# Performance work log

Hardware: AMD Instinct MI355X
Metric: run time of the kernel (lower is better)

Reference implementation:

```python
import jax, jax.numpy as jnp
import numpy as np

D_IN = 1024
D_OUT = 1024
SEQ = 4096


def setup_inputs() -> dict:
    key = jax.random.key(0)
    kx, kq, kk, kv = jax.random.split(key, 4)
    s = 1.0 / np.sqrt(D_IN)
    return {
        "x": jax.random.normal(kx, (SEQ, D_IN), dtype=jnp.float32),
        # torch Linear weights: shape [d_out, d_in], y = x @ W.T
        "Wq": jax.random.uniform(kq, (D_OUT, D_IN), jnp.float32, -s, s),
        "Wk": jax.random.uniform(kk, (D_OUT, D_IN), jnp.float32, -s, s),
        "Wv": jax.random.uniform(kv, (D_OUT, D_IN), jnp.float32, -s, s),
    }


def reference(x, Wq, Wk, Wv):
    # QKV projections (no bias)
    q = x @ Wq.T  # [N, d_out]
    k = x @ Wk.T
    v = x @ Wv.T
    scale = 1.0 / jnp.sqrt(jnp.asarray(k.shape[-1], x.dtype))
    att = jax.nn.softmax((q @ k.T) * scale, axis=-1)  # [N, N]
    return att @ v  # [N, d_out]
```

## Files before the change

### kernel.cpp

```cpp
#include <hip/hip_runtime.h>
#include <hip/hip_bf16.h>
#include <math.h>

typedef __attribute__((ext_vector_type(8))) short short8;
typedef __attribute__((ext_vector_type(4))) float floatx4;

static __device__ __forceinline__ unsigned short f2bf(float f) {
    union { float f; unsigned int u; } a; a.f = f;
    unsigned int u = a.u;
    return (unsigned short)((u + 0x7FFFu + ((u >> 16) & 1u)) >> 16);
}
static __device__ __forceinline__ float bf2f(unsigned short h) {
    union { unsigned int u; float f; } a; a.u = ((unsigned int)h) << 16;
    return a.f;
}

static __device__ __forceinline__ void cvt8(const float* __restrict__ src,
                                            unsigned short* __restrict__ dst, int i) {
    float4 v0 = *(const float4*)(src + i);
    float4 v1 = *(const float4*)(src + i + 4);
    ushort4 o0, o1;
    o0.x = f2bf(v0.x); o0.y = f2bf(v0.y); o0.z = f2bf(v0.z); o0.w = f2bf(v0.w);
    o1.x = f2bf(v1.x); o1.y = f2bf(v1.y); o1.z = f2bf(v1.z); o1.w = f2bf(v1.w);
    *(ushort4*)(dst + i) = o0;
    *(ushort4*)(dst + i + 4) = o1;
}

struct CV { const float* x; unsigned short* xb;
            const float* W[3]; unsigned short* Wb[3]; float* l; };
__global__ __launch_bounds__(256)
void cvt_all(CV a) {
    int b = blockIdx.x, t = threadIdx.x;
    if (b < 2048) {
        cvt8(a.x, a.xb, (b * 256 + t) * 8);
    } else if (b < 3584) {
        int z  = (b - 2048) >> 9;
        int bb = (b - 2048) & 511;
        cvt8(a.W[z], a.Wb[z], (bb * 256 + t) * 8);
    } else {
        float4 zz = {0.f, 0.f, 0.f, 0.f};
        #pragma unroll
        for (int c = 0; c < 4; c++)
            *(float4*)(a.l + t * 16 + c * 4) = zz;
    }
}

template<int BM, int BN, int BK, int TI, int TJ, int WCOLS>
__device__ __forceinline__ void gemm_core(const unsigned short* __restrict__ A,
                                          const unsigned short* __restrict__ B,
                                          int lda, int k_begin, int k_end,
                                          unsigned short* sA, unsigned short* sB,
                                          floatx4 (&acc)[TI][TJ],
                                          int bm, int bn)
{
    constexpr int CPR = BK / 8;
    constexpr int RPR = 2048 / BK;
    const int t    = threadIdx.x;
    const int wave = t >> 6;
    const int lane = t & 63;
    const int wm = (wave / WCOLS) * (TI * 16);
    const int wn = (wave % WCOLS) * (TJ * 16);

    const int srow   = t / CPR;
    const int schunk = t % CPR;
    const int gchunk = schunk ^ (srow & (CPR - 1));
    const int lm  = lane & 15;
    const int swz = lm & (CPR - 1);

    for (int k0 = k_begin; k0 < k_end; k0 += BK) {
        __syncthreads();
        #pragma unroll
        for (int r = 0; r < (BM * BK) / 2048; r++) {
            const unsigned short* gA =
                A + (size_t)(bm + srow + r * RPR) * lda + k0 + gchunk * 8;
            __builtin_amdgcn_global_load_lds(
                (const __attribute__((address_space(1))) void*)gA,
                (__attribute__((address_space(3))) void*)((char*)sA + wave * 1024 + r * 4096),
                16, 0, 0);
        }
        #pragma unroll
        for (int r = 0; r < (BN * BK) / 2048; r++) {
            const unsigned short* gB =
                B + (size_t)(bn + srow + r * RPR) * lda + k0 + gchunk * 8;
            __builtin_amdgcn_global_load_lds(
                (const __attribute__((address_space(1))) void*)gB,
                (__attribute__((address_space(3))) void*)((char*)sB + wave * 1024 + r * 4096),
                16, 0, 0);
        }
        __syncthreads();

        #pragma unroll
        for (int kk = 0; kk < BK; kk += 32) {
            const int c  = (kk >> 3) + (lane >> 4);
            const int ce = ((c ^ swz) << 3);
            short8 a_frag[TI], b_frag[TJ];
            #pragma unroll
            for (int i = 0; i < TI; i++)
                a_frag[i] = *(const short8*)&sA[(wm + i * 16 + lm) * BK + ce];
            #pragma unroll
            for (int j = 0; j < TJ; j++)
                b_frag[j] = *(const short8*)&sB[(wn + j * 16 + lm) * BK + ce];
            #pragma unroll
            for (int i = 0; i < TI; i++)
                #pragma unroll
                for (int j = 0; j < TJ; j++)
                    acc[i][j] = __builtin_amdgcn_mfma_f32_16x16x32_bf16(
                        a_frag[i], b_frag[j], acc[i][j], 0, 0, 0);
        }
    }
}


__device__ __forceinline__ void tile_store(unsigned short* sm,
                                           unsigned short (&vals)[4][4][4], int trans,
                                           unsigned short* __restrict__ C, int ldc,
                                           int rbase, int cbase)
{
    const int t = threadIdx.x, wave = t >> 6, lane = t & 63;
    const int wm = (wave >> 1) * 64, wn = (wave & 1) * 64;
    const int lm = lane & 15, rq = (lane >> 4) * 4;
    __syncthreads();
    #pragma unroll
    for (int i = 0; i < 4; i++)
        #pragma unroll
        for (int j = 0; j < 4; j++)
            #pragma unroll
            for (int r = 0; r < 4; r++) {
                int rr = trans ? (wn + j * 16 + lm) : (wm + i * 16 + rq + r);
                int cc = trans ? (wm + i * 16 + rq + r) : (wn + j * 16 + lm);
                sm[rr * 136 + cc] = vals[i][j][r];
            }
    __syncthreads();
    const int row = t >> 4, c16 = t & 15;
    #pragma unroll
    for (int p = 0; p < 8; p++) {
        int rr = p * 16 + row;
        short8 v = *(const short8*)&sm[rr * 136 + c16 * 8];
        *(short8*)&C[(size_t)(rbase + rr) * ldc + cbase + c16 * 8] = v;
    }
}

struct P3 { const unsigned short* W[3]; unsigned short* O[3]; };
__global__ __launch_bounds__(256)
void proj3(const unsigned short* __restrict__ xb, P3 a) {
    __shared__ unsigned short sm[2 * 128 * 128];
    unsigned short* sA = sm;
    unsigned short* sB = sm + 128 * 128;

    const int lid = blockIdx.x;
    const int xcd = lid & 7;
    const int rem = lid >> 3;
    const int row = (rem & 7) * 4 + (xcd >> 1);
    const int col = ((rem >> 3) & 3) * 2 + (xcd & 1);
    const int z   = rem >> 5;

    const unsigned short* B = a.W[z];
    unsigned short* O = a.O[z];
    const int trans = (z == 2);
    const float scale = (z == 0) ? 0.03125f : 1.0f;

    floatx4 acc[4][4];
    #pragma unroll
    for (int i = 0; i < 4; i++)
        #pragma unroll
        for (int j = 0; j < 4; j++) { floatx4 zz = {0.f,0.f,0.f,0.f}; acc[i][j] = zz; }

    const int bm = row * 128, bn = col * 128;
    gemm_core<128, 128, 128, 4, 4, 2>(xb, B, 1024, 0, 1024, sA, sB, acc, bm, bn);

    unsigned short vals[4][4][4];
    #pragma unroll
    for (int i = 0; i < 4; i++)
        #pragma unroll
        for (int j = 0; j < 4; j++)
            #pragma unroll
            for (int r = 0; r < 4; r++)
                vals[i][j][r] = f2bf(acc[i][j][r] * scale);

    tile_store(sm, vals, trans, O, trans ? 4096 : 1024,
               trans ? bn : bm, trans ? bm : bn);
}

__global__ __launch_bounds__(256)
void gemm_ps(const unsigned short* __restrict__ q, const unsigned short* __restrict__ k,
             unsigned short* __restrict__ Pm, float* __restrict__ l) {
    __shared__ unsigned short sm[2 * 128 * 128];
    unsigned short* sA = sm;
    unsigned short* sB = sm + 128 * 128;

    const int lid = blockIdx.x;
    const int xcd = lid & 7;
    const int i8  = lid >> 3;
    const int by  = (xcd & 1) * 16 + (i8 & 15);
    const int bx  = (xcd >> 1) * 8 + (i8 >> 4);

    floatx4 acc[4][4];
    #pragma unroll
    for (int i = 0; i < 4; i++)
        #pragma unroll
        for (int j = 0; j < 4; j++) { floatx4 zz = {0.f,0.f,0.f,0.f}; acc[i][j] = zz; }

    const int bm = by * 128, bn = bx * 128;
    gemm_core<128, 128, 128, 4, 4, 2>(q, k, 1024, 0, 1024, sA, sB, acc, bm, bn);

    const int lane = threadIdx.x & 63, wave = threadIdx.x >> 6;
    const int wm = (wave >> 1) * 64;
    const int lm = lane & 15, rq = (lane >> 4) * 4;
    unsigned short vals[4][4][4];
    #pragma unroll
    for (int i = 0; i < 4; i++) {
        #pragma unroll
        for (int r = 0; r < 4; r++) {
            int row = bm + wm + i * 16 + rq + r;
            float rs = 0.f;
            #pragma unroll
            for (int j = 0; j < 4; j++) {
                float e = __expf(acc[i][j][r]);
                rs += e;
                vals[i][j][r] = f2bf(e);
            }
            rs += __shfl_xor(rs, 1);
            rs += __shfl_xor(rs, 2);
            rs += __shfl_xor(rs, 4);
            rs += __shfl_xor(rs, 8);
            if (lm == 0) atomicAdd(l + row, rs);
        }
    }
    tile_store(sm, vals, 0, Pm, 4096, bm, bn);
}

__global__ __launch_bounds__(256)
void gemm_osplit(const unsigned short* __restrict__ Pm, const unsigned short* __restrict__ vT,
                 unsigned short* __restrict__ Opart) {
    __shared__ unsigned short sm[2 * 128 * 128];
    unsigned short* sA = sm;
    unsigned short* sB = sm + 128 * 128;

    const int lid = blockIdx.x;
    const int xcd = lid & 7;
    const int w   = lid >> 6;
    const int g   = (lid >> 3) & 7;
    const int s   = w * 8 + xcd;
    const int z   = s >> 5;
    const int row = s & 31;

    floatx4 acc[4][4];
    #pragma unroll
    for (int i = 0; i < 4; i++)
        #pragma unroll
        for (int j = 0; j < 4; j++) { floatx4 zz = {0.f,0.f,0.f,0.f}; acc[i][j] = zz; }

    const int bm = row * 128, bn = g * 128;
    gemm_core<128, 128, 128, 4, 4, 2>(Pm, vT, 4096, z * 2048, (z + 1) * 2048,
                                      sA, sB, acc, bm, bn);

    unsigned short vals[4][4][4];
    #pragma unroll
    for (int i = 0; i < 4; i++)
        #pragma unroll
        for (int j = 0; j < 4; j++)
            #pragma unroll
            for (int r = 0; r < 4; r++)
                vals[i][j][r] = f2bf(acc[i][j][r]);

    tile_store(sm, vals, 0, Opart + (size_t)z * (4096 * 1024), 1024, bm, bn);
}

__global__ __launch_bounds__(256)
void reduce_scale(const unsigned short* __restrict__ Op, const float* __restrict__ l,
                  float* __restrict__ out) {
    int i = (blockIdx.x * 256 + threadIdx.x) * 4;
    ushort4 a = *(const ushort4*)(Op + i);
    ushort4 b = *(const ushort4*)(Op + 4096 * 1024 + i);
    float inv = 1.0f / l[i >> 10];
    float4 o;
    o.x = (bf2f(a.x) + bf2f(b.x)) * inv;
    o.y = (bf2f(a.y) + bf2f(b.y)) * inv;
    o.z = (bf2f(a.z) + bf2f(b.z)) * inv;
    o.w = (bf2f(a.w) + bf2f(b.w)) * inv;
    *(float4*)(out + i) = o;
}

extern "C" void kernel_launch(void* const* d_in, const int* in_sizes, int n_in,
                              void* d_out, int out_size, void* d_ws, size_t ws_size,
                              hipStream_t stream) {
    const float* x  = (const float*)d_in[0];
    const float* Wq = (const float*)d_in[1];
    const float* Wk = (const float*)d_in[2];
    const float* Wv = (const float*)d_in[3];
    float* out = (float*)d_out;

    const int SEQ = 4096, D = 1024;
    char* ws = (char*)d_ws;
    const size_t MB = 1u << 20;
    unsigned short* vTb = (unsigned short*)(ws);
    unsigned short* xb  = (unsigned short*)(ws + 8 * MB);
    unsigned short* Wqb = (unsigned short*)(ws + 16 * MB);
    unsigned short* Wkb = (unsigned short*)(ws + 18 * MB);
    unsigned short* Wvb = (unsigned short*)(ws + 20 * MB);
    unsigned short* qb  = (unsigned short*)(ws + 22 * MB);
    unsigned short* kb  = (unsigned short*)(ws + 30 * MB);
    unsigned short* P   = (unsigned short*)(ws + 38 * MB);
    float*          l   = (float*)(ws + 70 * MB);
    unsigned short* Opart = (unsigned short*)(ws + 72 * MB);

    dim3 blk(256);
    CV cv = {x, xb, {Wq, Wk, Wv}, {Wqb, Wkb, Wvb}, l};
    cvt_all<<<dim3(3585), blk, 0, stream>>>(cv);

    P3 p3 = {{Wqb, Wkb, Wvb}, {qb, kb, vTb}};
    proj3<<<dim3(768), blk, 0, stream>>>(xb, p3);

    gemm_ps<<<dim3(1024), blk, 0, stream>>>(qb, kb, P, l);

    gemm_osplit<<<dim3(512), blk, 0, stream>>>(P, vTb, Opart);

    reduce_scale<<<(SEQ * D) / 1024, blk, 0, stream>>>(Opart, l, out);
}
```

Baseline: 204.2 us.

## Move GEMMs to 256x256 tiles with pipelined LDS prefetch and 4-way split-K

Replaces the 128x128 single-buffered GEMM core with a 256x256 tile core run by 512 threads. It stages half-tiles into double-buffered LDS ahead of use, interleaves prefetch with MFMA work under barriers, and raises wave priority during MFMA sections. The projection, score and output GEMMs all use this core. The output GEMM changes from 2-way to 4-way split-K, the reduction kernel sums four partials, and the partials reuse dead workspace regions. The aim is higher arithmetic intensity per byte loaded and hidden global-load latency. The cost is a large LDS footprint, high register pressure, fewer blocks per kernel, and extra partial-sum traffic in the reduction.

New measurement: 201.1 us. Within noise of the previous version (-1.5%).

```diff
diff --git a/kernel.cpp b/kernel.cpp
--- a/kernel.cpp
+++ b/kernel.cpp
@@ -45,225 +45,224 @@
     }
 }
 
-template<int BM, int BN, int BK, int TI, int TJ, int WCOLS>
-__device__ __forceinline__ void gemm_core(const unsigned short* __restrict__ A,
-                                          const unsigned short* __restrict__ B,
-                                          int lda, int k_begin, int k_end,
-                                          unsigned short* sA, unsigned short* sB,
-                                          floatx4 (&acc)[TI][TJ],
-                                          int bm, int bn)
+__device__ __forceinline__ void gemm256_core(
+    const unsigned short* __restrict__ A, const unsigned short* __restrict__ B,
+    int lda, int k_begin, int bm, int bn,
+    unsigned short* lds, floatx4 (&acc)[8][4])
 {
-    constexpr int CPR = BK / 8;
-    constexpr int RPR = 2048 / BK;
     const int t    = threadIdx.x;
     const int wave = t >> 6;
     const int lane = t & 63;
-    const int wm = (wave / WCOLS) * (TI * 16);
-    const int wn = (wave % WCOLS) * (TJ * 16);
-
-    const int srow   = t / CPR;
-    const int schunk = t % CPR;
-    const int gchunk = schunk ^ (srow & (CPR - 1));
-    const int lm  = lane & 15;
-    const int swz = lm & (CPR - 1);
-
-    for (int k0 = k_begin; k0 < k_end; k0 += BK) {
+    const int wrow = wave >> 2;
+    const int wcol = wave & 3;
+    const int lm   = lane & 15;
+    const int ce8  = (((lane >> 4) ^ ((lm >> 1) & 3)) << 3);
+
+    const int srow = t >> 2;
+    const int gsh  = (((t & 3) ^ ((srow >> 1) & 3)) << 3);
+    const unsigned short* srcA = A + (size_t)(bm + srow) * lda + k_begin + gsh;
+    const unsigned short* srcB = B + (size_t)(bn + srow) * lda + k_begin + gsh;
+    const size_t rstep = (size_t)128 * lda;
+    char* ldsc = (char*)lds;
+    const int w1k = wave << 10;
+
+    const int aoff = ((wrow << 7) + lm) * 32 + ce8;
+    const int boff = 32768 + ((wcol << 6) + lm) * 32 + ce8;
+
+#define STAGE(kind, kh, tau) do {                                              \
+        int taue_ = (tau) >= 16 ? (tau) - 2 : (tau);   \
+        int ko_ = (taue_ << 6) + ((kh) << 5);                                  \
+        unsigned lo_ = ((kind) << 16) + (((tau) & 1) << 15) + ((kh) << 14) + w1k; \
+        const unsigned short* s_ = ((kind) ? srcB : srcA) + ko_;               \
+        __builtin_amdgcn_global_load_lds(                                      \
+            (const __attribute__((address_space(1))) void*)s_,                 \
+            (__attribute__((address_space(3))) void*)(ldsc + lo_), 16, 0, 0);  \
+        __builtin_amdgcn_global_load_lds(                                      \
+            (const __attribute__((address_space(1))) void*)(s_ + rstep),       \
+            (__attribute__((address_space(3))) void*)(ldsc + lo_ + 8192), 16, 0, 0); \
+    } while (0)
+
+    STAGE(1, 0, 0); STAGE(0, 0, 0); STAGE(1, 1, 0); STAGE(0, 1, 0);
+    STAGE(1, 0, 1); STAGE(0, 0, 1); STAGE(1, 1, 1);
+    asm volatile("s_waitcnt vmcnt(6)" ::: "memory");
+    __builtin_amdgcn_s_barrier();
+
+    short8 a4[4], b4[4];
+    for (int t2 = 0; t2 < 16; t2 += 2) {
+        #pragma unroll
+        for (int s = 0; s < 8; s++) {
+            const int tc = t2 + (s >> 2);
+            const int s4 = s & 3;
+            const int ks = s4 >> 1, ih = s4 & 1;
+            const int base = ((tc & 1) << 14) + (ks << 13);
+            #pragma unroll
+            for (int ii = 0; ii < 4; ii++)
+                a4[ii] = *(const short8*)&lds[base + aoff + ((ih * 4 + ii) << 9)];
+            if (s4 == 0 || s4 == 2) {
+                #pragma unroll
+                for (int j = 0; j < 4; j++)
+                    b4[j] = *(const short8*)&lds[base + boff + (j << 9)];
+            }
+            if      (s4 == 0) STAGE(0, 1, tc + 1);
+            else if (s4 == 1) STAGE(1, 0, tc + 2);
+            else if (s4 == 2) STAGE(0, 0, tc + 2);
+            else              STAGE(1, 1, tc + 2);
+            __builtin_amdgcn_s_barrier();
+            asm volatile("s_waitcnt lgkmcnt(0)" ::: "memory");
+            __builtin_amdgcn_sched_barrier(0);
+            __builtin_amdgcn_s_setprio(1);
+            #pragma unroll
+            for (int ii = 0; ii < 4; ii++)
+                #pragma unroll
+                for (int j = 0; j < 4; j++)
+                    acc[ih * 4 + ii][j] = __builtin_amdgcn_mfma_f32_16x16x32_bf16(
+                        a4[ii], b4[j], acc[ih * 4 + ii][j], 0, 0, 0);
+            __builtin_amdgcn_s_setprio(0);
+            if (s4 == 3) asm volatile("s_waitcnt vmcnt(6)" ::: "memory");
+            __builtin_amdgcn_s_barrier();
+        }
+    }
+#undef STAGE
+}
+
+__device__ __forceinline__ void tile_store256(unsigned short* sm,
+                                              floatx4 (&acc)[8][4], float scale, int trans,
+                                              unsigned short* __restrict__ C, int ldc,
+                                              int rbase, int cbase)
+{
+    const int t = threadIdx.x, wave = t >> 6, lane = t & 63;
+    const int wrow = wave >> 2, wcol = wave & 3;
+    const int lm = lane & 15, rq = ((lane >> 4) << 2);
+    #pragma unroll
+    for (int h = 0; h < 2; h++) {
         __syncthreads();
-        #pragma unroll
-        for (int r = 0; r < (BM * BK) / 2048; r++) {
-            const unsigned short* gA =
-                A + (size_t)(bm + srow + r * RPR) * lda + k0 + gchunk * 8;
-            __builtin_amdgcn_global_load_lds(
-                (const __attribute__((address_space(1))) void*)gA,
-                (__attribute__((address_space(3))) void*)((char*)sA + wave * 1024 + r * 4096),
-                16, 0, 0);
-        }
-        #pragma unroll
-        for (int r = 0; r < (BN * BK) / 2048; r++) {
-            const unsigned short* gB =
-                B + (size_t)(bn + srow + r * RPR) * lda + k0 + gchunk * 8;
-            __builtin_amdgcn_global_load_lds(
-                (const __attribute__((address_space(1))) void*)gB,
-                (__attribute__((address_space(3))) void*)((char*)sB + wave * 1024 + r * 4096),
-                16, 0, 0);
+        if (!trans) {
+            if (wrow == h) {
+                #pragma unroll
+                for (int i = 0; i < 8; i++)
+                    #pragma unroll
+                    for (int j = 0; j < 4; j++)
+                        #pragma unroll
+                        for (int r = 0; r < 4; r++)
+                            sm[(i * 16 + rq + r) * 264 + wcol * 64 + j * 16 + lm] =
+                                f2bf(acc[i][j][r] * scale);
+            }
+        } else {
+            if ((wcol >> 1) == h) {
+                #pragma unroll
+                for (int i = 0; i < 8; i++)
+                    #pragma unroll
+                    for (int j = 0; j < 4; j++) {
+                        ushort4 v;
+                        v.x = f2bf(acc[i][j][0] * scale);
+                        v.y = f2bf(acc[i][j][1] * scale);
+                        v.z = f2bf(acc[i][j][2] * scale);
+                        v.w = f2bf(acc[i][j][3] * scale);
+                        *(ushort4*)&sm[((wcol & 1) * 64 + j * 16 + lm) * 264 +
+                                       wrow * 128 + i * 16 + rq] = v;
+                    }
+            }
         }
         __syncthreads();
-
-        #pragma unroll
-        for (int kk = 0; kk < BK; kk += 32) {
-            const int c  = (kk >> 3) + (lane >> 4);
-            const int ce = ((c ^ swz) << 3);
-            short8 a_frag[TI], b_frag[TJ];
-            #pragma unroll
-            for (int i = 0; i < TI; i++)
-                a_frag[i] = *(const short8*)&sA[(wm + i * 16 + lm) * BK + ce];
-            #pragma unroll
-            for (int j = 0; j < TJ; j++)
-                b_frag[j] = *(const short8*)&sB[(wn + j * 16 + lm) * BK + ce];
-            #pragma unroll
-            for (int i = 0; i < TI; i++)
-                #pragma unroll
-                for (int j = 0; j < TJ; j++)
-                    acc[i][j] = __builtin_amdgcn_mfma_f32_16x16x32_bf16(
-                        a_frag[i], b_frag[j], acc[i][j], 0, 0, 0);
+        #pragma unroll
+        for (int p = 0; p < 4; p++) {
+            int row = p * 32 + (t >> 4);
+            int c0  = (t & 15) * 8;
+            *(short8*)&C[(size_t)(rbase + h * 128 + row) * ldc + cbase + c0] =
+                *(const short8*)&sm[row * 264 + c0];
+            *(short8*)&C[(size_t)(rbase + h * 128 + row) * ldc + cbase + c0 + 128] =
+                *(const short8*)&sm[row * 264 + c0 + 128];
         }
     }
 }
 
-
-__device__ __forceinline__ void tile_store(unsigned short* sm,
-                                           unsigned short (&vals)[4][4][4], int trans,
-                                           unsigned short* __restrict__ C, int ldc,
-                                           int rbase, int cbase)
-{
-    const int t = threadIdx.x, wave = t >> 6, lane = t & 63;
-    const int wm = (wave >> 1) * 64, wn = (wave & 1) * 64;
-    const int lm = lane & 15, rq = (lane >> 4) * 4;
-    __syncthreads();
-    #pragma unroll
-    for (int i = 0; i < 4; i++)
-        #pragma unroll
-        for (int j = 0; j < 4; j++)
-            #pragma unroll
-            for (int r = 0; r < 4; r++) {
-                int rr = trans ? (wn + j * 16 + lm) : (wm + i * 16 + rq + r);
-                int cc = trans ? (wm + i * 16 + rq + r) : (wn + j * 16 + lm);
-                sm[rr * 136 + cc] = vals[i][j][r];
-            }
-    __syncthreads();
-    const int row = t >> 4, c16 = t & 15;
-    #pragma unroll
-    for (int p = 0; p < 8; p++) {
-        int rr = p * 16 + row;
-        short8 v = *(const short8*)&sm[rr * 136 + c16 * 8];
-        *(short8*)&C[(size_t)(rbase + rr) * ldc + cbase + c16 * 8] = v;
-    }
-}
-
 struct P3 { const unsigned short* W[3]; unsigned short* O[3]; };
-__global__ __launch_bounds__(256)
+__global__ __launch_bounds__(512, 2)
 void proj3(const unsigned short* __restrict__ xb, P3 a) {
-    __shared__ unsigned short sm[2 * 128 * 128];
-    unsigned short* sA = sm;
-    unsigned short* sB = sm + 128 * 128;
-
+    __shared__ __align__(16) unsigned short lds[65536];
     const int lid = blockIdx.x;
-    const int xcd = lid & 7;
-    const int rem = lid >> 3;
-    const int row = (rem & 7) * 4 + (xcd >> 1);
-    const int col = ((rem >> 3) & 3) * 2 + (xcd & 1);
-    const int z   = rem >> 5;
-
-    const unsigned short* B = a.W[z];
-    unsigned short* O = a.O[z];
+    const int xcd = lid & 7, rem = lid >> 3;
+    const int z   = rem >> 3;
+    const int idx = xcd * 8 + (rem & 7);
+    const int by = idx >> 2, bx = idx & 3;
+    const int bm = by * 256, bn = bx * 256;
+
+    floatx4 acc[8][4];
+    #pragma unroll
+    for (int i = 0; i < 8; i++)
+        #pragma unroll
+        for (int j = 0; j < 4; j++) { floatx4 zz = {0.f,0.f,0.f,0.f}; acc[i][j] = zz; }
+
+    gemm256_core(xb, a.W[z], 1024, 0, bm, bn, lds, acc);
+
     const int trans = (z == 2);
     const float scale = (z == 0) ? 0.03125f : 1.0f;
-
-    floatx4 acc[4][4];
-    #pragma unroll
-    for (int i = 0; i < 4; i++)
-        #pragma unroll
-        for (int j = 0; j < 4; j++) { floatx4 zz = {0.f,0.f,0.f,0.f}; acc[i][j] = zz; }
-
-    const int bm = row * 128, bn = col * 128;
-    gemm_core<128, 128, 128, 4, 4, 2>(xb, B, 1024, 0, 1024, sA, sB, acc, bm, bn);
-
-    unsigned short vals[4][4][4];
-    #pragma unroll
-    for (int i = 0; i < 4; i++)
-        #pragma unroll
-        for (int j = 0; j < 4; j++)
-            #pragma unroll
-            for (int r = 0; r < 4; r++)
-                vals[i][j][r] = f2bf(acc[i][j][r] * scale);
-
-    tile_store(sm, vals, trans, O, trans ? 4096 : 1024,
-               trans ? bn : bm, trans ? bm : bn);
-}
-
-__global__ __launch_bounds__(256)
+    tile_store256(lds, acc, scale, trans, a.O[z],
+                  trans ? 4096 : 1024, trans ? bn : bm, trans ? bm : bn);
+}
+
+__global__ __launch_bounds__(512, 2)
 void gemm_ps(const unsigned short* __restrict__ q, const unsigned short* __restrict__ k,
              unsigned short* __restrict__ Pm, float* __restrict__ l) {
-    __shared__ unsigned short sm[2 * 128 * 128];
-    unsigned short* sA = sm;
-    unsigned short* sB = sm + 128 * 128;
-
+    __shared__ __align__(16) unsigned short lds[65536];
     const int lid = blockIdx.x;
-    const int xcd = lid & 7;
-    const int i8  = lid >> 3;
-    const int by  = (xcd & 1) * 16 + (i8 & 15);
-    const int bx  = (xcd >> 1) * 8 + (i8 >> 4);
-
-    floatx4 acc[4][4];
-    #pragma unroll
-    for (int i = 0; i < 4; i++)
+    const int xcd = lid & 7, r32 = lid >> 3;
+    const int by = ((xcd >> 1) << 2) + (r32 & 3);
+    const int bx = ((xcd & 1) << 3) + (r32 >> 2);
+    const int bm = by * 256, bn = bx * 256;
+
+    floatx4 acc[8][4];
+    #pragma unroll
+    for (int i = 0; i < 8; i++)
         #pragma unroll
         for (int j = 0; j < 4; j++) { floatx4 zz = {0.f,0.f,0.f,0.f}; acc[i][j] = zz; }
 
-    const int bm = by * 128, bn = bx * 128;
-    gemm_core<128, 128, 128, 4, 4, 2>(q, k, 1024, 0, 1024, sA, sB, acc, bm, bn);
+    gemm256_core(q, k, 1024, 0, bm, bn, lds, acc);
 
     const int lane = threadIdx.x & 63, wave = threadIdx.x >> 6;
-    const int wm = (wave >> 1) * 64;
-    const int lm = lane & 15, rq = (lane >> 4) * 4;
-    unsigned short vals[4][4][4];
-    #pragma unroll
-    for (int i = 0; i < 4; i++) {
+    const int wrow = wave >> 2;
+    const int lm = lane & 15, rq = ((lane >> 4) << 2);
+    #pragma unroll
+    for (int i = 0; i < 8; i++) {
         #pragma unroll
         for (int r = 0; r < 4; r++) {
-            int row = bm + wm + i * 16 + rq + r;
             float rs = 0.f;
             #pragma unroll
             for (int j = 0; j < 4; j++) {
                 float e = __expf(acc[i][j][r]);
+                acc[i][j][r] = e;
                 rs += e;
-                vals[i][j][r] = f2bf(e);
             }
             rs += __shfl_xor(rs, 1);
             rs += __shfl_xor(rs, 2);
             rs += __shfl_xor(rs, 4);
             rs += __shfl_xor(rs, 8);
-            if (lm == 0) atomicAdd(l + row, rs);
+            if (lm == 0) atomicAdd(l + bm + wrow * 128 + i * 16 + rq + r, rs);
         }
     }
-    tile_store(sm, vals, 0, Pm, 4096, bm, bn);
-}
-
-__global__ __launch_bounds__(256)
+    tile_store256(lds, acc, 1.0f, 0, Pm, 4096, bm, bn);
+}
+
+__global__ __launch_bounds__(512, 2)
 void gemm_osplit(const unsigned short* __restrict__ Pm, const unsigned short* __restrict__ vT,
                  unsigned short* __restrict__ Opart) {
-    __shared__ unsigned short sm[2 * 128 * 128];
-    unsigned short* sA = sm;
-    unsigned short* sB = sm + 128 * 128;
-
+    __shared__ __align__(16) unsigned short lds[65536];
     const int lid = blockIdx.x;
-    const int xcd = lid & 7;
-    const int w   = lid >> 6;
-    const int g   = (lid >> 3) & 7;
-    const int s   = w * 8 + xcd;
-    const int z   = s >> 5;
-    const int row = s & 31;
-
-    floatx4 acc[4][4];
-    #pragma unroll
-    for (int i = 0; i < 4; i++)
+    const int xcd = lid & 7, r32 = lid >> 3;
+    const int z   = r32 & 3;
+    const int idx = (r32 >> 2) * 8 + xcd;
+    const int by = idx >> 2, bx = idx & 3;
+
+    floatx4 acc[8][4];
+    #pragma unroll
+    for (int i = 0; i < 8; i++)
         #pragma unroll
         for (int j = 0; j < 4; j++) { floatx4 zz = {0.f,0.f,0.f,0.f}; acc[i][j] = zz; }
 
-    const int bm = row * 128, bn = g * 128;
-    gemm_core<128, 128, 128, 4, 4, 2>(Pm, vT, 4096, z * 2048, (z + 1) * 2048,
-                                      sA, sB, acc, bm, bn);
-
-    unsigned short vals[4][4][4];
-    #pragma unroll
-    for (int i = 0; i < 4; i++)
-        #pragma unroll
-        for (int j = 0; j < 4; j++)
-            #pragma unroll
-            for (int r = 0; r < 4; r++)
-                vals[i][j][r] = f2bf(acc[i][j][r]);
-
-    tile_store(sm, vals, 0, Opart + (size_t)z * (4096 * 1024), 1024, bm, bn);
+    gemm256_core(Pm, vT, 4096, z * 1024, by * 256, bx * 256, lds, acc);
+
+    tile_store256(lds, acc, 1.0f, 0, Opart + (size_t)z * (4096 * 1024), 1024,
+                  by * 256, bx * 256);
 }
 
 __global__ __launch_bounds__(256)
@@ -271,13 +270,15 @@
                   float* __restrict__ out) {
     int i = (blockIdx.x * 256 + threadIdx.x) * 4;
     ushort4 a = *(const ushort4*)(Op + i);
-    ushort4 b = *(const ushort4*)(Op + 4096 * 1024 + i);
+    ushort4 b = *(const ushort4*)(Op + 4194304 + i);
+    ushort4 c = *(const ushort4*)(Op + 8388608 + i);
+    ushort4 d = *(const ushort4*)(Op + 12582912 + i);
     float inv = 1.0f / l[i >> 10];
     float4 o;
-    o.x = (bf2f(a.x) + bf2f(b.x)) * inv;
-    o.y = (bf2f(a.y) + bf2f(b.y)) * inv;
-    o.z = (bf2f(a.z) + bf2f(b.z)) * inv;
-    o.w = (bf2f(a.w) + bf2f(b.w)) * inv;
+    o.x = (bf2f(a.x) + bf2f(b.x) + bf2f(c.x) + bf2f(d.x)) * inv;
+    o.y = (bf2f(a.y) + bf2f(b.y) + bf2f(c.y) + bf2f(d.y)) * inv;
+    o.z = (bf2f(a.z) + bf2f(b.z) + bf2f(c.z) + bf2f(d.z)) * inv;
+    o.w = (bf2f(a.w) + bf2f(b.w) + bf2f(c.w) + bf2f(d.w)) * inv;
     *(float4*)(out + i) = o;
 }
 
@@ -290,7 +291,6 @@
     const float* Wv = (const float*)d_in[3];
     float* out = (float*)d_out;
 
-    const int SEQ = 4096, D = 1024;
     char* ws = (char*)d_ws;
     const size_t MB = 1u << 20;
     unsigned short* vTb = (unsigned short*)(ws);
@@ -300,20 +300,20 @@
     unsigned short* Wvb = (unsigned short*)(ws + 20 * MB);
     unsigned short* qb  = (unsigned short*)(ws + 22 * MB);
     unsigned short* kb  = (unsigned short*)(ws + 30 * MB);
-    unsigned short* P   = (unsigned short*)(ws + 38 * MB);
-    float*          l   = (float*)(ws + 70 * MB);
-    unsigned short* Opart = (unsigned short*)(ws + 72 * MB);
-
-    dim3 blk(256);
+    unsigned short* P   = (unsigned short*)(ws + 40 * MB);
+    float*          l   = (float*)(ws + 72 * MB);
+    unsigned short* Opart = (unsigned short*)(ws + 8 * MB);
+
+    dim3 b256(256), b512(512);
     CV cv = {x, xb, {Wq, Wk, Wv}, {Wqb, Wkb, Wvb}, l};
-    cvt_all<<<dim3(3585), blk, 0, stream>>>(cv);
+    cvt_all<<<dim3(3585), b256, 0, stream>>>(cv);
 
     P3 p3 = {{Wqb, Wkb, Wvb}, {qb, kb, vTb}};
-    proj3<<<dim3(768), blk, 0, stream>>>(xb, p3);
-
-    gemm_ps<<<dim3(1024), blk, 0, stream>>>(qb, kb, P, l);
-
-    gemm_osplit<<<dim3(512), blk, 0, stream>>>(P, vTb, Opart);
-
-    reduce_scale<<<(SEQ * D) / 1024, blk, 0, stream>>>(Opart, l, out);
-}
+    proj3<<<dim3(192), b512, 0, stream>>>(xb, p3);
+
+    gemm_ps<<<dim3(256), b512, 0, stream>>>(qb, kb, P, l);
+
+    gemm_osplit<<<dim3(256), b512, 0, stream>>>(P, vTb, Opart);
+
+    reduce_scale<<<dim3(4096), b256, 0, stream>>>(Opart, l, out);
+}
```
